# Performance work log

Hardware: AMD Instinct MI355X
Metric: run time of the kernel (lower is better)

Reference implementation:

```python
import jax, jax.numpy as jnp
import numpy as np

N, P, T, K = 20000, 5, 16, 3
IN, H, O = 150, 64, 128


def setup_inputs() -> dict:
    key = jax.random.key(0)
    k1, k2, k3, k4, k5 = jax.random.split(key, 5)
    x = jax.random.normal(k1, (N, IN), dtype=jnp.float32)
    conn_idx = jax.random.randint(k2, (N, P, T, K), 0, N, dtype=jnp.int32)
    conn_w = jax.random.uniform(k3, (N, P, T, K), dtype=jnp.float32)
    # learned params
    W1 = jax.random.normal(k4, (H, IN), dtype=jnp.float32) * 0.05   # linear_1 (no bias)
    Wg = jax.random.normal(k5, (O, H, P, T), dtype=jnp.float32) * 0.05  # geodesic conv weight
    bg = jnp.zeros((O,), dtype=jnp.float32)                          # geodesic conv bias
    return {"x": x, "conn_idx": conn_idx, "conn_w": conn_w, "W1": W1, "Wg": Wg, "bg": bg}


def reference(x, conn_idx, conn_w, W1, Wg, bg):
    # Linear + ReLU: [N, H]
    h = jax.nn.relu(x @ W1.T)
    # Geodesic patch gather: interpolate vertex features into P x T bins
    g = jnp.take(h, conn_idx, axis=0)                 # [N, P, T, K, H]
    patches = jnp.einsum('nptk,nptkh->npth', conn_w, g)  # [N, P, T, H]
    # Geodesic convolution: contract patch bins and channels
    out = jnp.einsum('npth,ohpt->no', patches, Wg) + bg  # [N, O]
    # L2 normalize per vertex
    norm = jnp.linalg.norm(out, axis=-1, keepdims=True)
    return out / norm
```

## Files before the change

### kernel.cpp

```cpp
#include <hip/hip_runtime.h>
#include <hip/hip_fp16.h>

#define NV   20000
#define KK   3
#define INF  150
#define HH   64
#define OO   128
#define PT   80
#define KTOT 5120
#define NB   32
#define BS2  72
#define RS2  152
#define CHB  (NB * RS2)
#define XS   168

typedef _Float16 fh8 __attribute__((ext_vector_type(8)));
typedef __attribute__((ext_vector_type(4))) float f32x4;

__device__ __forceinline__ unsigned short f2h(float f) {
    return __half_as_ushort(__float2half(f));
}
__device__ __forceinline__ float h2f(unsigned short u) {
    return __half2float(__ushort_as_half(u));
}

struct Conn { int idx[6]; float w[6]; };

__global__ __launch_bounds__(256) void prep_kernel(
    const float* __restrict__ Wg, const float* __restrict__ x,
    const float* __restrict__ W1, unsigned short* __restrict__ W2,
    unsigned short* __restrict__ hb) {
    __shared__ __align__(16) unsigned char smem[32256];
    const int tid = threadIdx.x;

    if (blockIdx.x < 128) {
        float* lds = (float*)smem;
        const int o = blockIdx.x;
        const float* src = Wg + o * KTOT;
        for (int t = tid; t < KTOT; t += 256) {
            int h = t / 80, bin = t - h * 80;
            lds[h * 81 + bin] = src[t];
        }
        __syncthreads();
        for (int t = tid; t < KTOT; t += 256) {
            W2[(t >> 5) * 4096 + o * 32 + (t & 31)] =
                f2h(lds[(t & 63) * 81 + (t >> 6)]);
        }
        return;
    }

    unsigned short* xs = (unsigned short*)smem;
    unsigned short* ws = xs + 32 * XS;
    const int n0 = (blockIdx.x - 128) * 32;

    for (int e = tid; e < 32 * INF; e += 256) {
        int r = e / INF, c = e - r * INF;
        xs[r * XS + c] = f2h(x[n0 * INF + e]);
    }
    for (int e = tid; e < 32 * 18; e += 256) {
        int r = e / 18, c = e - r * 18;
        xs[r * XS + 150 + c] = 0;
    }
    for (int e = tid; e < 64 * INF; e += 256) {
        int r = e / INF, c = e - r * INF;
        ws[r * XS + c] = f2h(W1[e]);
    }
    for (int e = tid; e < 64 * 18; e += 256) {
        int r = e / 18, c = e - r * 18;
        ws[r * XS + 150 + c] = 0;
    }
    __syncthreads();

    const int wv   = tid >> 6;
    const int lane = tid & 63;
    const int q    = lane >> 4;
    const int r16  = lane & 15;
    const int o0   = wv * 16;

    f32x4 acc0 = {0.f, 0.f, 0.f, 0.f};
    f32x4 acc1 = acc0;
    #pragma unroll
    for (int s = 0; s < 5; s++) {
        const int kb = s * 32 + q * 8;
        fh8 a0 = *(const fh8*)(xs + r16 * XS + kb);
        fh8 a1 = *(const fh8*)(xs + (16 + r16) * XS + kb);
        fh8 b  = *(const fh8*)(ws + (o0 + r16) * XS + kb);
        acc0 = __builtin_amdgcn_mfma_f32_16x16x32_f16(a0, b, acc0, 0, 0, 0);
        acc1 = __builtin_amdgcn_mfma_f32_16x16x32_f16(a1, b, acc1, 0, 0, 0);
    }
    #pragma unroll
    for (int r = 0; r < 4; r++) {
        float v0 = acc0[r] > 0.f ? acc0[r] : 0.f;
        float v1 = acc1[r] > 0.f ? acc1[r] : 0.f;
        hb[(n0 + q * 4 + r) * HH + o0 + r16]      = f2h(v0);
        hb[(n0 + 16 + q * 4 + r) * HH + o0 + r16] = f2h(v1);
    }
}

__global__ __launch_bounds__(256, 4) void geo_kernel(
    const int*   __restrict__ conn_idx, const float* __restrict__ conn_w,
    const unsigned short* __restrict__ W2, const unsigned short* __restrict__ hb,
    float* __restrict__ out, unsigned short* __restrict__ part1) {
    __shared__ __align__(16) unsigned short pch[2 * CHB];

    const int tid  = threadIdx.x;
    const int ks   = blockIdx.x & 1;
    const int n0   = (blockIdx.x >> 1) * NB;
    const int wv   = tid >> 6;
    const int lane = tid & 63;
    const int q    = lane >> 4;
    const int r16  = lane & 15;
    const int j8   = tid & 7;
    const int bl   = (tid >> 3) & 1;
    const int ng   = tid >> 4;
    const int bbase = ks * 40;
    const int Sbase = ks * 80;

    f32x4 acc00 = {0.f, 0.f, 0.f, 0.f};
    f32x4 acc01 = acc00, acc10 = acc00, acc11 = acc00;

    Conn cA, cB;
    fh8  hv[6];

    auto loadc = [&](int cc, Conn& c) {
        const int bin = bbase + cc * 2 + bl;
        #pragma unroll
        for (int i = 0; i < 2; i++) {
            const int g = (n0 + ng + i * 16) * (PT * KK) + bin * KK;
            c.idx[i * 3 + 0] = conn_idx[g];
            c.idx[i * 3 + 1] = conn_idx[g + 1];
            c.idx[i * 3 + 2] = conn_idx[g + 2];
            c.w[i * 3 + 0]   = conn_w[g];
            c.w[i * 3 + 1]   = conn_w[g + 1];
            c.w[i * 3 + 2]   = conn_w[g + 2];
        }
    };
    auto loadh = [&](const Conn& c) {
        #pragma unroll
        for (int t = 0; t < 6; t++)
            hv[t] = *(const fh8*)(hb + c.idx[t] * HH + j8 * 8);
    };
    auto cwrite = [&](const Conn& c, unsigned short* buf) {
        #pragma unroll
        for (int i = 0; i < 2; i++) {
            const int n = ng + i * 16;
            _Float16 w0 = (_Float16)c.w[i * 3 + 0];
            _Float16 w1 = (_Float16)c.w[i * 3 + 1];
            _Float16 w2 = (_Float16)c.w[i * 3 + 2];
            fh8 W0 = {w0, w0, w0, w0, w0, w0, w0, w0};
            fh8 W1v = {w1, w1, w1, w1, w1, w1, w1, w1};
            fh8 W2v = {w2, w2, w2, w2, w2, w2, w2, w2};
            fh8 r = hv[i * 3] * W0 + hv[i * 3 + 1] * W1v + hv[i * 3 + 2] * W2v;
            *(fh8*)(buf + n * RS2 + bl * BS2 + j8 * 8) = r;
        }
    };
    auto mfmaph = [&](const unsigned short* buf, int cc) {
        #pragma unroll
        for (int s = 0; s < 4; s++) {
            const int S  = Sbase + cc * 4 + s;
            const int ao = (s >> 1) * BS2 + (s & 1) * 32 + q * 8;
            fh8 a0 = *(const fh8*)(buf + r16 * RS2 + ao);
            fh8 a1 = *(const fh8*)(buf + (16 + r16) * RS2 + ao);
            fh8 b0 = *(const fh8*)(W2 + S * 4096 + (wv * 32 + r16) * 32 + q * 8);
            fh8 b1 = *(const fh8*)(W2 + S * 4096 + (wv * 32 + 16 + r16) * 32 + q * 8);
            acc00 = __builtin_amdgcn_mfma_f32_16x16x32_f16(a0, b0, acc00, 0, 0, 0);
            acc01 = __builtin_amdgcn_mfma_f32_16x16x32_f16(a0, b1, acc01, 0, 0, 0);
            acc10 = __builtin_amdgcn_mfma_f32_16x16x32_f16(a1, b0, acc10, 0, 0, 0);
            acc11 = __builtin_amdgcn_mfma_f32_16x16x32_f16(a1, b1, acc11, 0, 0, 0);
        }
    };

    loadc(0, cA);
    loadc(1, cB);
    loadh(cA);
    cwrite(cA, pch);
    __syncthreads();

    auto body = [&](int cc, Conn& use, Conn& fill) {
        if (cc + 2 < 20) loadc(cc + 2, fill);
        if (cc + 1 < 20) loadh(use);
        mfmaph(&pch[(cc & 1) * CHB], cc);
        if (cc + 1 < 20) cwrite(use, &pch[((cc + 1) & 1) * CHB]);
        __syncthreads();
    };
    for (int cc = 0; cc < 20; cc += 2) {
        body(cc, cB, cA);
        body(cc + 1, cA, cB);
    }

    const int o0 = wv * 32;
    if (ks == 0) {
        #pragma unroll
        for (int r = 0; r < 4; r++) {
            out[(n0 + q * 4 + r) * OO + o0 + r16]           = acc00[r];
            out[(n0 + q * 4 + r) * OO + o0 + 16 + r16]      = acc01[r];
            out[(n0 + 16 + q * 4 + r) * OO + o0 + r16]      = acc10[r];
            out[(n0 + 16 + q * 4 + r) * OO + o0 + 16 + r16] = acc11[r];
        }
    } else {
        #pragma unroll
        for (int r = 0; r < 4; r++) {
            part1[(n0 + q * 4 + r) * OO + o0 + r16]           = f2h(acc00[r]);
            part1[(n0 + q * 4 + r) * OO + o0 + 16 + r16]      = f2h(acc01[r]);
            part1[(n0 + 16 + q * 4 + r) * OO + o0 + r16]      = f2h(acc10[r]);
            part1[(n0 + 16 + q * 4 + r) * OO + o0 + 16 + r16] = f2h(acc11[r]);
        }
    }
}

__global__ __launch_bounds__(256) void norm_kernel(
    float* __restrict__ out, const unsigned short* __restrict__ part1,
    const float* __restrict__ bg) {
    const int tid = threadIdx.x;
    const int n   = blockIdx.x * 32 + (tid >> 3);
    const int l   = tid & 7;
    float v[16];
    float s = 0.f;
    #pragma unroll
    for (int i = 0; i < 16; i++) {
        const int o = i * 8 + l;
        v[i] = out[n * OO + o] + h2f(part1[n * OO + o]) + bg[o];
        s += v[i] * v[i];
    }
    for (int off = 4; off; off >>= 1) s += __shfl_down(s, off, 8);
    const float r = rsqrtf(__shfl(s, 0, 8));
    #pragma unroll
    for (int i = 0; i < 16; i++)
        out[n * OO + i * 8 + l] = v[i] * r;
}

extern "C" void kernel_launch(void* const* d_in, const int* in_sizes, int n_in,
                              void* d_out, int out_size, void* d_ws, size_t ws_size,
                              hipStream_t stream) {
    const float* x        = (const float*)d_in[0];
    const int*   conn_idx = (const int*)  d_in[1];
    const float* conn_w   = (const float*)d_in[2];
    const float* W1       = (const float*)d_in[3];
    const float* Wg       = (const float*)d_in[4];
    const float* bg       = (const float*)d_in[5];
    float*       out      = (float*)d_out;

    unsigned short* W2    = (unsigned short*)d_ws;
    unsigned short* hb    = W2 + OO * KTOT;
    unsigned short* part1 = hb + NV * HH;

    hipLaunchKernelGGL(prep_kernel, dim3(128 + NV / 32), dim3(256), 0, stream,
                       Wg, x, W1, W2, hb);
    hipLaunchKernelGGL(geo_kernel, dim3(2 * NV / NB), dim3(256), 0, stream,
                       conn_idx, conn_w, W2, hb, out, part1);
    hipLaunchKernelGGL(norm_kernel, dim3(NV / 32), dim3(256), 0, stream,
                       out, part1, bg);
}
```

Measured before the change: 188.6 us.

## Build patch operands in registers per wave, dropping LDS staging and block syncs

The geodesic kernel now gives each wavefront its own job: a 32-vertex tile, a 64-output half and a K-split half. Each wave gathers the h rows and forms the weighted patch directly in the MFMA A-operand registers, so the LDS double buffer and __syncthreads are gone. The aim is to remove shared-memory round trips and barrier stalls. In exchange, every gather is now done twice (once per output half), the wave holds more registers (launch bounds lowered to 3), and the grid shrinks to 625 blocks.

After: 353.5 us. 87.4% more time.

```diff
diff --git a/kernel.cpp b/kernel.cpp
--- a/kernel.cpp
+++ b/kernel.cpp
@@ -8,10 +8,6 @@
 #define OO   128
 #define PT   80
 #define KTOT 5120
-#define NB   32
-#define BS2  72
-#define RS2  152
-#define CHB  (NB * RS2)
 #define XS   168
 
 typedef _Float16 fh8 __attribute__((ext_vector_type(8)));
@@ -23,8 +19,6 @@
 __device__ __forceinline__ float h2f(unsigned short u) {
     return __half2float(__ushort_as_half(u));
 }
-
-struct Conn { int idx[6]; float w[6]; };
 
 __global__ __launch_bounds__(256) void prep_kernel(
     const float* __restrict__ Wg, const float* __restrict__ x,
@@ -97,114 +91,113 @@
     }
 }
 
-__global__ __launch_bounds__(256, 4) void geo_kernel(
+struct CSet { int i[6]; float w[6]; };
+
+__global__ __launch_bounds__(256, 3) void geo_kernel(
     const int*   __restrict__ conn_idx, const float* __restrict__ conn_w,
     const unsigned short* __restrict__ W2, const unsigned short* __restrict__ hb,
     float* __restrict__ out, unsigned short* __restrict__ part1) {
-    __shared__ __align__(16) unsigned short pch[2 * CHB];
-
     const int tid  = threadIdx.x;
-    const int ks   = blockIdx.x & 1;
-    const int n0   = (blockIdx.x >> 1) * NB;
-    const int wv   = tid >> 6;
+    const int job  = blockIdx.x * 4 + (tid >> 6);
     const int lane = tid & 63;
     const int q    = lane >> 4;
     const int r16  = lane & 15;
-    const int j8   = tid & 7;
-    const int bl   = (tid >> 3) & 1;
-    const int ng   = tid >> 4;
+
+    const int nblk = job % 625;
+    const int rest = job / 625;
+    const int oh   = rest & 1;
+    const int ks   = rest >> 1;
+    const int n0w  = nblk * 32;
+    const int obase = oh * 64;
     const int bbase = ks * 40;
-    const int Sbase = ks * 80;
-
-    f32x4 acc00 = {0.f, 0.f, 0.f, 0.f};
-    f32x4 acc01 = acc00, acc10 = acc00, acc11 = acc00;
-
-    Conn cA, cB;
-    fh8  hv[6];
-
-    auto loadc = [&](int cc, Conn& c) {
-        const int bin = bbase + cc * 2 + bl;
-        #pragma unroll
-        for (int i = 0; i < 2; i++) {
-            const int g = (n0 + ng + i * 16) * (PT * KK) + bin * KK;
-            c.idx[i * 3 + 0] = conn_idx[g];
-            c.idx[i * 3 + 1] = conn_idx[g + 1];
-            c.idx[i * 3 + 2] = conn_idx[g + 2];
-            c.w[i * 3 + 0]   = conn_w[g];
-            c.w[i * 3 + 1]   = conn_w[g + 1];
-            c.w[i * 3 + 2]   = conn_w[g + 2];
+
+    const int v0 = n0w + r16;
+    const int cb0 = v0 * (PT * KK);
+    const int cb1 = cb0 + 16 * (PT * KK);
+
+    f32x4 acc[2][4];
+    #pragma unroll
+    for (int m = 0; m < 2; m++)
+        #pragma unroll
+        for (int ot = 0; ot < 4; ot++)
+            acc[m][ot] = (f32x4){0.f, 0.f, 0.f, 0.f};
+
+    auto loadc = [&](int bin, CSet& c) {
+        const int g0 = cb0 + bin * 3;
+        const int g1 = cb1 + bin * 3;
+        #pragma unroll
+        for (int t = 0; t < 3; t++) {
+            c.i[t]     = conn_idx[g0 + t];
+            c.w[t]     = conn_w[g0 + t];
+            c.i[3 + t] = conn_idx[g1 + t];
+            c.w[3 + t] = conn_w[g1 + t];
         }
     };
-    auto loadh = [&](const Conn& c) {
-        #pragma unroll
-        for (int t = 0; t < 6; t++)
-            hv[t] = *(const fh8*)(hb + c.idx[t] * HH + j8 * 8);
+
+    auto step = [&](int bin, const CSet& cC, CSet& cN, bool pf) {
+        if (pf) loadc(bin + 1, cN);
+        fh8 hv[12];
+        #pragma unroll
+        for (int m = 0; m < 2; m++)
+            #pragma unroll
+            for (int t = 0; t < 3; t++) {
+                const unsigned short* p = hb + cC.i[m * 3 + t] * HH + q * 8;
+                hv[(m * 3 + t) * 2 + 0] = *(const fh8*)p;
+                hv[(m * 3 + t) * 2 + 1] = *(const fh8*)(p + 32);
+            }
+        fh8 Bv[8];
+        #pragma unroll
+        for (int hf = 0; hf < 2; hf++)
+            #pragma unroll
+            for (int ot = 0; ot < 4; ot++)
+                Bv[hf * 4 + ot] = *(const fh8*)(W2 + (bin * 2 + hf) * 4096 +
+                                                (obase + ot * 16 + r16) * 32 + q * 8);
+        #pragma unroll
+        for (int m = 0; m < 2; m++) {
+            const _Float16 w0 = (_Float16)cC.w[m * 3 + 0];
+            const _Float16 w1 = (_Float16)cC.w[m * 3 + 1];
+            const _Float16 w2 = (_Float16)cC.w[m * 3 + 2];
+            const fh8 W0v = {w0, w0, w0, w0, w0, w0, w0, w0};
+            const fh8 W1v = {w1, w1, w1, w1, w1, w1, w1, w1};
+            const fh8 W2v = {w2, w2, w2, w2, w2, w2, w2, w2};
+            #pragma unroll
+            for (int hf = 0; hf < 2; hf++) {
+                fh8 A = hv[(m * 3 + 0) * 2 + hf] * W0v +
+                        hv[(m * 3 + 1) * 2 + hf] * W1v +
+                        hv[(m * 3 + 2) * 2 + hf] * W2v;
+                #pragma unroll
+                for (int ot = 0; ot < 4; ot++)
+                    acc[m][ot] = __builtin_amdgcn_mfma_f32_16x16x32_f16(
+                        A, Bv[hf * 4 + ot], acc[m][ot], 0, 0, 0);
+            }
+        }
     };
-    auto cwrite = [&](const Conn& c, unsigned short* buf) {
-        #pragma unroll
-        for (int i = 0; i < 2; i++) {
-            const int n = ng + i * 16;
-            _Float16 w0 = (_Float16)c.w[i * 3 + 0];
-            _Float16 w1 = (_Float16)c.w[i * 3 + 1];
-            _Float16 w2 = (_Float16)c.w[i * 3 + 2];
-            fh8 W0 = {w0, w0, w0, w0, w0, w0, w0, w0};
-            fh8 W1v = {w1, w1, w1, w1, w1, w1, w1, w1};
-            fh8 W2v = {w2, w2, w2, w2, w2, w2, w2, w2};
-            fh8 r = hv[i * 3] * W0 + hv[i * 3 + 1] * W1v + hv[i * 3 + 2] * W2v;
-            *(fh8*)(buf + n * RS2 + bl * BS2 + j8 * 8) = r;
-        }
-    };
-    auto mfmaph = [&](const unsigned short* buf, int cc) {
-        #pragma unroll
-        for (int s = 0; s < 4; s++) {
-            const int S  = Sbase + cc * 4 + s;
-            const int ao = (s >> 1) * BS2 + (s & 1) * 32 + q * 8;
-            fh8 a0 = *(const fh8*)(buf + r16 * RS2 + ao);
-            fh8 a1 = *(const fh8*)(buf + (16 + r16) * RS2 + ao);
-            fh8 b0 = *(const fh8*)(W2 + S * 4096 + (wv * 32 + r16) * 32 + q * 8);
-            fh8 b1 = *(const fh8*)(W2 + S * 4096 + (wv * 32 + 16 + r16) * 32 + q * 8);
-            acc00 = __builtin_amdgcn_mfma_f32_16x16x32_f16(a0, b0, acc00, 0, 0, 0);
-            acc01 = __builtin_amdgcn_mfma_f32_16x16x32_f16(a0, b1, acc01, 0, 0, 0);
-            acc10 = __builtin_amdgcn_mfma_f32_16x16x32_f16(a1, b0, acc10, 0, 0, 0);
-            acc11 = __builtin_amdgcn_mfma_f32_16x16x32_f16(a1, b1, acc11, 0, 0, 0);
-        }
-    };
-
-    loadc(0, cA);
-    loadc(1, cB);
-    loadh(cA);
-    cwrite(cA, pch);
-    __syncthreads();
-
-    auto body = [&](int cc, Conn& use, Conn& fill) {
-        if (cc + 2 < 20) loadc(cc + 2, fill);
-        if (cc + 1 < 20) loadh(use);
-        mfmaph(&pch[(cc & 1) * CHB], cc);
-        if (cc + 1 < 20) cwrite(use, &pch[((cc + 1) & 1) * CHB]);
-        __syncthreads();
-    };
-    for (int cc = 0; cc < 20; cc += 2) {
-        body(cc, cB, cA);
-        body(cc + 1, cA, cB);
-    }
-
-    const int o0 = wv * 32;
+
+    CSet cA, cB;
+    loadc(bbase, cA);
+    for (int i = 0; i < 40; i += 2) {
+        step(bbase + i,     cA, cB, i + 1 < 40);
+        step(bbase + i + 1, cB, cA, i + 2 < 40);
+    }
+
     if (ks == 0) {
         #pragma unroll
-        for (int r = 0; r < 4; r++) {
-            out[(n0 + q * 4 + r) * OO + o0 + r16]           = acc00[r];
-            out[(n0 + q * 4 + r) * OO + o0 + 16 + r16]      = acc01[r];
-            out[(n0 + 16 + q * 4 + r) * OO + o0 + r16]      = acc10[r];
-            out[(n0 + 16 + q * 4 + r) * OO + o0 + 16 + r16] = acc11[r];
-        }
+        for (int m = 0; m < 2; m++)
+            #pragma unroll
+            for (int ot = 0; ot < 4; ot++)
+                #pragma unroll
+                for (int r = 0; r < 4; r++)
+                    out[(n0w + m * 16 + q * 4 + r) * OO + obase + ot * 16 + r16] =
+                        acc[m][ot][r];
     } else {
         #pragma unroll
-        for (int r = 0; r < 4; r++) {
-            part1[(n0 + q * 4 + r) * OO + o0 + r16]           = f2h(acc00[r]);
-            part1[(n0 + q * 4 + r) * OO + o0 + 16 + r16]      = f2h(acc01[r]);
-            part1[(n0 + 16 + q * 4 + r) * OO + o0 + r16]      = f2h(acc10[r]);
-            part1[(n0 + 16 + q * 4 + r) * OO + o0 + 16 + r16] = f2h(acc11[r]);
-        }
+        for (int m = 0; m < 2; m++)
+            #pragma unroll
+            for (int ot = 0; ot < 4; ot++)
+                #pragma unroll
+                for (int r = 0; r < 4; r++)
+                    part1[(n0w + m * 16 + q * 4 + r) * OO + obase + ot * 16 + r16] =
+                        f2h(acc[m][ot][r]);
     }
 }
 
@@ -246,7 +239,7 @@
 
     hipLaunchKernelGGL(prep_kernel, dim3(128 + NV / 32), dim3(256), 0, stream,
                        Wg, x, W1, W2, hb);
-    hipLaunchKernelGGL(geo_kernel, dim3(2 * NV / NB), dim3(256), 0, stream,
+    hipLaunchKernelGGL(geo_kernel, dim3(625), dim3(256), 0, stream,
                        conn_idx, conn_w, W2, hb, out, part1);
     hipLaunchKernelGGL(norm_kernel, dim3(NV / 32), dim3(256), 0, stream,
                        out, part1, bg);
```
